# Performance work log

Measured on AMD Instinct MI355X. Metric: run time of the kernel, lower is better.

## Reference

```python
import jax, jax.numpy as jnp
import numpy as np


def gcn_conv(x, W, b, src, dst):
    """PyG-style GCNConv: add self-loops, symmetric normalization, then scatter-add."""
    n = x.shape[0]
    loop = jnp.arange(n, dtype=src.dtype)
    s = jnp.concatenate([src, loop])  # [E+N]
    d = jnp.concatenate([dst, loop])
    deg = jax.ops.segment_sum(jnp.ones(s.shape[0], dtype=x.dtype), d, num_segments=n)
    dinv = jax.lax.rsqrt(jnp.maximum(deg, 1.0))  # deg >= 1 due to self-loops
    norm = dinv[s] * dinv[d]                     # [E+N]
    h = x @ W                                    # [N, out]
    msg = h[s] * norm[:, None]                   # gather + scale
    return jax.ops.segment_sum(msg, d, num_segments=n) + b


def setup_inputs() -> dict:
    key = jax.random.key(0)
    ks = jax.random.split(key, 8)
    N, E, IN, H, C = 50000, 800000, 128, 64, 16
    x = jax.random.normal(ks[0], (N, IN), dtype=jnp.float32)
    edge_index = jax.random.randint(ks[1], (2, E), 0, N, dtype=jnp.int32)
    def glorot(k, shp):
        fan_in, fan_out = shp
        lim = (6.0 / (fan_in + fan_out)) ** 0.5
        return jax.random.uniform(k, shp, jnp.float32, -lim, lim)
    return {
        "x": x,
        "edge_index": edge_index,
        "W1": glorot(ks[2], (IN, H)), "b1": jnp.zeros((H,), jnp.float32),
        "W2": glorot(ks[3], (H, H)),  "b2": jnp.zeros((H,), jnp.float32),
        "Wm1": glorot(ks[4], (2 * H, H)), "bm1": jnp.zeros((H,), jnp.float32),
        "Wm2": glorot(ks[5], (H, C)),     "bm2": jnp.zeros((C,), jnp.float32),
    }


def reference(x, edge_index, W1, b1, W2, b2, Wm1, bm1, Wm2, bm2):
    src, dst = edge_index[0], edge_index[1]
    h = jax.nn.relu(gcn_conv(x, W1, b1, src, dst))
    # dropout is identity in eval mode
    h = jax.nn.relu(gcn_conv(h, W2, b2, src, dst))
    ef = jnp.concatenate([h[src], h[dst]], axis=1)  # [E, 2H]
    z = jax.nn.relu(ef @ Wm1 + bm1)
    return z @ Wm2 + bm2  # [E, numClasses]
```

## Files before the change

### kernel.cpp

```cpp
#include <hip/hip_runtime.h>
#include <hip/hip_bf16.h>

__global__ __launch_bounds__(256) void k_deg(const int* __restrict__ dst, int* __restrict__ deg, int E) {
    int e = blockIdx.x * 256 + threadIdx.x;
    if (e < E) atomicAdd(&deg[dst[e]], 1);
}

__global__ __launch_bounds__(256) void k_dinv(const int* __restrict__ deg, float* __restrict__ dinv, int N) {
    int n = blockIdx.x * 256 + threadIdx.x;
    if (n < N) dinv[n] = rsqrtf((float)(deg[n] + 1));
}

__global__ __launch_bounds__(256) void k_scan_sum(const int* __restrict__ deg, int* __restrict__ bsum, int N) {
    int n = blockIdx.x * 256 + threadIdx.x;
    int v = (n < N) ? deg[n] : 0;
#pragma unroll
    for (int o = 32; o > 0; o >>= 1) v += __shfl_down(v, o, 64);
    __shared__ int sh[4];
    if ((threadIdx.x & 63) == 0) sh[threadIdx.x >> 6] = v;
    __syncthreads();
    if (threadIdx.x == 0) bsum[blockIdx.x] = sh[0] + sh[1] + sh[2] + sh[3];
}

__global__ __launch_bounds__(256) void k_scan_off(int* __restrict__ bsum, int nb) {
    __shared__ int sh[256];
    int t = threadIdx.x;
    sh[t] = (t < nb) ? bsum[t] : 0;
    __syncthreads();
    for (int o = 1; o < 256; o <<= 1) {
        int y = (t >= o) ? sh[t - o] : 0;
        __syncthreads();
        sh[t] += y;
        __syncthreads();
    }
    if (t < nb) bsum[t] = (t == 0) ? 0 : sh[t - 1];
}

__global__ __launch_bounds__(256) void k_scan_write(const int* __restrict__ deg, const int* __restrict__ boff,
                                                    int* __restrict__ row_start, int* __restrict__ cursor, int N) {
    int n = blockIdx.x * 256 + threadIdx.x;
    int t = threadIdx.x, lane = t & 63, w = t >> 6;
    int v = (n < N) ? deg[n] : 0;
    int x = v;
#pragma unroll
    for (int o = 1; o < 64; o <<= 1) {
        int y = __shfl_up(x, o, 64);
        if (lane >= o) x += y;
    }
    __shared__ int wsum[4];
    if (lane == 63) wsum[w] = x;
    __syncthreads();
    int wo = 0;
#pragma unroll
    for (int i = 0; i < 4; ++i) wo += (i < w) ? wsum[i] : 0;
    int excl = boff[blockIdx.x] + wo + x - v;
    if (n < N) { row_start[n] = excl; cursor[n] = excl; }
    if (n == N - 1) row_start[N] = excl + v;
}

template <bool PAIR>
__global__ __launch_bounds__(256) void k_fill(const int* __restrict__ src, const int* __restrict__ dst,
                                              int* __restrict__ cursor, void* __restrict__ item, int E) {
    int e = blockIdx.x * 256 + threadIdx.x;
    if (e < E) {
        int d = dst[e];
        int pos = atomicAdd(&cursor[d], 1);
        if (PAIR) ((int2*)item)[pos] = make_int2(src[e], e);
        else      ((int*)item)[pos] = e;
    }
}

__global__ __launch_bounds__(256) void k_dvec(const int* __restrict__ rowst, int* __restrict__ dvec, int N) {
    int w = threadIdx.x >> 6, lane = threadIdx.x & 63;
    int d = blockIdx.x * 4 + w;
    if (d >= N) return;
    int beg = rowst[d], end = rowst[d + 1];
    for (int k = beg + lane; k < end; k += 64) dvec[k] = d;
}

__global__ __launch_bounds__(256) void k_tr(const float* __restrict__ in, float* __restrict__ outp, int R, int C) {
    int i = blockIdx.x * 256 + threadIdx.x;
    if (i < R * C) {
        int r = i / C, c = i % C;
        outp[(size_t)c * R + r] = in[(size_t)r * C + c];
    }
}

__global__ __launch_bounds__(256) void k_wpq(const float* __restrict__ Wm1, float* __restrict__ WPQ) {
    int i = blockIdx.x * 256 + threadIdx.x;
    if (i < 128 * 64) {
        int j = i >> 6, k = i & 63;
        WPQ[i] = (j < 64) ? Wm1[k * 64 + j] : Wm1[(64 + k) * 64 + (j - 64)];
    }
}

template <int K, bool RELU, bool BIAS, bool SCALE>
__global__ __launch_bounds__(256) void k_mm_slice(const float* __restrict__ X,
                                                  const float* __restrict__ WT,
                                                  const float* __restrict__ bias,
                                                  const float* __restrict__ dinv,
                                                  float* __restrict__ Y, int N) {
    int n = blockIdx.x * 256 + threadIdx.x;
    int j0 = blockIdx.y * 16;
    int nc = n < N ? n : N - 1;
    const float* xr = X + (size_t)nc * K;
    const float* wr = WT + (size_t)j0 * K;
    float acc[16];
#pragma unroll
    for (int j = 0; j < 16; ++j) acc[j] = BIAS ? bias[j0 + j] : 0.f;
#pragma unroll 1
    for (int k0 = 0; k0 < K; k0 += 8) {
        float ef[8];
        *(float4*)(ef)     = *(const float4*)(xr + k0);
        *(float4*)(ef + 4) = *(const float4*)(xr + k0 + 4);
        if (RELU) {
#pragma unroll
            for (int kk = 0; kk < 8; ++kk) ef[kk] = fmaxf(ef[kk], 0.f);
        }
#pragma unroll
        for (int j = 0; j < 16; ++j) {
#pragma unroll
            for (int kk = 0; kk < 8; ++kk)
                acc[j] = fmaf(ef[kk], wr[j * K + k0 + kk], acc[j]);
        }
    }
    if (n < N) {
        if (SCALE) {
            float dn = dinv[n];
#pragma unroll
            for (int j = 0; j < 16; ++j) acc[j] *= dn;
        }
        float4* yp = (float4*)(Y + (size_t)n * 64 + j0);
#pragma unroll
        for (int q = 0; q < 4; ++q) yp[q] = *(float4*)(acc + q * 4);
    }
}

__global__ __launch_bounds__(256) void k_pq_slice(const float* __restrict__ A2,
                                                  const float* __restrict__ WPQ,
                                                  const float* __restrict__ bm1,
                                                  float* __restrict__ Pb, float* __restrict__ Qb, int N) {
    int n = blockIdx.x * 256 + threadIdx.x;
    int j0g = blockIdx.y * 16;
    bool isP = j0g < 64;
    int jo = isP ? j0g : j0g - 64;
    float* Y = isP ? Pb : Qb;
    int nc = n < N ? n : N - 1;
    const float* xr = A2 + (size_t)nc * 64;
    const float* wr = WPQ + (size_t)j0g * 64;
    float acc[16];
#pragma unroll
    for (int j = 0; j < 16; ++j) acc[j] = isP ? bm1[jo + j] : 0.f;
#pragma unroll 1
    for (int k0 = 0; k0 < 64; k0 += 8) {
        float ef[8];
        *(float4*)(ef)     = *(const float4*)(xr + k0);
        *(float4*)(ef + 4) = *(const float4*)(xr + k0 + 4);
#pragma unroll
        for (int kk = 0; kk < 8; ++kk) ef[kk] = fmaxf(ef[kk], 0.f);
#pragma unroll
        for (int j = 0; j < 16; ++j)
#pragma unroll
            for (int kk = 0; kk < 8; ++kk)
                acc[j] = fmaf(ef[kk], wr[j * 64 + k0 + kk], acc[j]);
    }
    if (n < N) {
        float4* yp = (float4*)(Y + (size_t)n * 64 + jo);
#pragma unroll
        for (int q = 0; q < 4; ++q) yp[q] = *(float4*)(acc + q * 4);
    }
}

template <bool PAIR>
__global__ __launch_bounds__(256) void k_gather(const float* __restrict__ hs, const float* __restrict__ dinv,
                                                const int* __restrict__ row_start, const void* __restrict__ item,
                                                const int* __restrict__ srcArr,
                                                const float* __restrict__ bias,
                                                float* __restrict__ a, int N) {
    int w = threadIdx.x >> 6, lane = threadIdx.x & 63;
    int d = blockIdx.x * 4 + w;
    if (d >= N) return;
    int beg = row_start[d], end = row_start[d + 1];
    float dd = dinv[d];
    float acc = hs[(size_t)d * 64 + lane];
    int k = beg;
    for (; k + 8 <= end; k += 8) {
        int ss[8];
        if (PAIR) {
            const int2* it = (const int2*)item;
#pragma unroll
            for (int u = 0; u < 8; ++u) ss[u] = it[k + u].x;
        } else {
            const int* eid = (const int*)item;
            int ee[8];
#pragma unroll
            for (int u = 0; u < 8; ++u) ee[u] = eid[k + u];
#pragma unroll
            for (int u = 0; u < 8; ++u) ss[u] = srcArr[ee[u]];
        }
        float v[8];
#pragma unroll
        for (int u = 0; u < 8; ++u) v[u] = hs[(size_t)ss[u] * 64 + lane];
#pragma unroll
        for (int u = 0; u < 8; ++u) acc += v[u];
    }
    for (; k < end; ++k) {
        int s = PAIR ? ((const int2*)item)[k].x : srcArr[((const int*)item)[k]];
        acc += hs[(size_t)s * 64 + lane];
    }
    a[(size_t)d * 64 + lane] = fmaf(acc, dd, bias[lane]);
}

__global__ __launch_bounds__(256) void k_p_inplace(float* __restrict__ A2P,
                                                   const float* __restrict__ WPQ,
                                                   const float* __restrict__ bm1, int N) {
    int n = blockIdx.x * 256 + threadIdx.x;
    int nc = n < N ? n : N - 1;
    const float* xr = A2P + (size_t)nc * 64;
    float acc[64];
#pragma unroll
    for (int j = 0; j < 64; ++j) acc[j] = bm1[j];
#pragma unroll 1
    for (int k0 = 0; k0 < 64; k0 += 8) {
        float ef[8];
        *(float4*)(ef)     = *(const float4*)(xr + k0);
        *(float4*)(ef + 4) = *(const float4*)(xr + k0 + 4);
#pragma unroll
        for (int kk = 0; kk < 8; ++kk) ef[kk] = fmaxf(ef[kk], 0.f);
#pragma unroll
        for (int j = 0; j < 64; ++j)
#pragma unroll
            for (int kk = 0; kk < 8; ++kk)
                acc[j] = fmaf(ef[kk], WPQ[j * 64 + k0 + kk], acc[j]);
    }
    if (n < N) {
#pragma unroll
        for (int q = 0; q < 16; ++q)
            *(float4*)(A2P + (size_t)n * 64 + q * 4) = *(float4*)(acc + q * 4);
    }
}

__global__ __launch_bounds__(256) void k_edge_pq(const float* __restrict__ P,
                                                 const float* __restrict__ Q,
                                                 const int* __restrict__ src,
                                                 const int* __restrict__ dst,
                                                 const float* __restrict__ W2T,
                                                 const float* __restrict__ bm2,
                                                 float* __restrict__ out, int E) {
    int e = blockIdx.x * 256 + threadIdx.x;
    int ec = e < E ? e : E - 1;
    int s = src[ec], d = dst[ec];
    const float4* p4 = (const float4*)(P + (size_t)s * 64);
    const float4* q4 = (const float4*)(Q + (size_t)d * 64);
    float z[64];
#pragma unroll
    for (int c = 0; c < 16; ++c) {
        float4 a = p4[c], b = q4[c];
        z[c * 4 + 0] = fmaxf(a.x + b.x, 0.f);
        z[c * 4 + 1] = fmaxf(a.y + b.y, 0.f);
        z[c * 4 + 2] = fmaxf(a.z + b.z, 0.f);
        z[c * 4 + 3] = fmaxf(a.w + b.w, 0.f);
    }
    float o[16];
#pragma unroll
    for (int c = 0; c < 16; ++c) {
        float a = bm2[c];
#pragma unroll
        for (int j = 0; j < 64; ++j) a = fmaf(z[j], W2T[c * 64 + j], a);
        o[c] = a;
    }
    if (e < E) {
        float4* op = (float4*)(out + (size_t)e * 16);
#pragma unroll
        for (int q = 0; q < 4; ++q) op[q] = *(float4*)(o + q * 4);
    }
}

template <bool PAIR>
__global__ __launch_bounds__(256) void k_edge_csr(const float* __restrict__ P,
                                                  const float* __restrict__ Q,
                                                  const int* __restrict__ dvec,
                                                  const void* __restrict__ item,
                                                  const int* __restrict__ srcArr,
                                                  const float* __restrict__ W2T,
                                                  const float* __restrict__ bm2,
                                                  float* __restrict__ out, int E) {
    int i = blockIdx.x * 256 + threadIdx.x;
    int ic = i < E ? i : E - 1;
    int s, e;
    if (PAIR) {
        int2 pe = ((const int2*)item)[ic];
        s = pe.x; e = pe.y;
    } else {
        e = ((const int*)item)[ic];
        s = srcArr[e];
    }
    int d = dvec[ic];
    const float4* p4 = (const float4*)(P + (size_t)s * 64);
    const float4* q4 = (const float4*)(Q + (size_t)d * 64);
    float o[16];
#pragma unroll
    for (int t = 0; t < 16; ++t) o[t] = bm2[t];
#pragma unroll
    for (int c = 0; c < 16; ++c) {
        float4 a = p4[c], b = q4[c];
        float z0 = fmaxf(a.x + b.x, 0.f);
        float z1 = fmaxf(a.y + b.y, 0.f);
        float z2 = fmaxf(a.z + b.z, 0.f);
        float z3 = fmaxf(a.w + b.w, 0.f);
#pragma unroll
        for (int t = 0; t < 16; ++t) {
            o[t] = fmaf(z0, W2T[t * 64 + c * 4 + 0], o[t]);
            o[t] = fmaf(z1, W2T[t * 64 + c * 4 + 1], o[t]);
            o[t] = fmaf(z2, W2T[t * 64 + c * 4 + 2], o[t]);
            o[t] = fmaf(z3, W2T[t * 64 + c * 4 + 3], o[t]);
        }
    }
    if (i < E) {
        float4* op = (float4*)(out + (size_t)e * 16);
#pragma unroll
        for (int q = 0; q < 4; ++q) op[q] = *(float4*)(o + q * 4);
    }
}

extern "C" void kernel_launch(void* const* d_in, const int* in_sizes, int n_in,
                              void* d_out, int out_size, void* d_ws, size_t ws_size,
                              hipStream_t stream) {
    const float* x   = (const float*)d_in[0];
    const int* ei    = (const int*)d_in[1];
    const float* W1  = (const float*)d_in[2];
    const float* b1  = (const float*)d_in[3];
    const float* W2  = (const float*)d_in[4];
    const float* b2  = (const float*)d_in[5];
    const float* Wm1 = (const float*)d_in[6];
    const float* bm1 = (const float*)d_in[7];
    const float* Wm2 = (const float*)d_in[8];
    const float* bm2 = (const float*)d_in[9];
    float* out = (float*)d_out;

    const int H  = in_sizes[3];
    const int IN = in_sizes[2] / H;
    const int N  = in_sizes[0] / IN;
    const int E  = in_sizes[1] / 2;
    const int* src = ei;
    const int* dst = ei + E;

    auto al = [](size_t b) { return (b + 255) & ~(size_t)255; };
    char* ws = (char*)d_ws;

    const size_t wb     = al((size_t)IN * H * 4) + al((size_t)H * H * 4) + al((size_t)2 * H * H * 4) + al((size_t)H * 16 * 4);
    const size_t rowstB = al(((size_t)N + 1) * 4);
    const size_t nodeB  = al((size_t)N * 64 * 4);
    const size_t pairB  = al((size_t)E * 8);
    const size_t eidB   = al((size_t)E * 4);
    const size_t needA  = wb + rowstB + pairB + 3 * nodeB;
    const size_t needB  = wb + rowstB + eidB  + 3 * nodeB;

    const int tier = (needA <= ws_size) ? 0 : (needB <= ws_size) ? 1 : 2;

    float *W1T, *W2T, *WPQ, *Wm2T, *bufB, *Qbuf, *Pbuf, *dinv;
    int *deg, *rowst, *cursor, *bsum;
    void* item;
    float* bufA = (float*)d_out;
    bool slicedP = true;

    size_t off = 0;
    auto alc = [&](size_t b) { void* p = ws + off; off += al(b); return p; };

    if (tier <= 1) {
        W1T  = (float*)alc((size_t)IN * H * 4);
        W2T  = (float*)alc((size_t)H * H * 4);
        WPQ  = (float*)alc((size_t)2 * H * H * 4);
        Wm2T = (float*)alc((size_t)H * 16 * 4);
        rowst = (int*)alc(((size_t)N + 1) * 4);
        item  = alc(tier == 0 ? (size_t)E * 8 : (size_t)E * 4);
        bufB = (float*)alc((size_t)N * 64 * 4);
        Qbuf = (float*)alc((size_t)N * 64 * 4);
        Pbuf = (float*)alc((size_t)N * 64 * 4);
        char* pz = (char*)Pbuf;
        dinv   = (float*)pz;
        deg    = (int*)(pz + al((size_t)N * 4));
        cursor = (int*)(pz + 2 * al((size_t)N * 4));
        bsum   = (int*)(pz + 3 * al((size_t)N * 4));
    } else {
        dinv = (float*)alc((size_t)N * 4);
        W1T  = (float*)alc((size_t)IN * H * 4);
        W2T  = (float*)alc((size_t)H * H * 4);
        WPQ  = (float*)alc((size_t)2 * H * H * 4);
        Wm2T = (float*)alc((size_t)H * 16 * 4);
        bufB = (float*)alc((size_t)N * 64 * 4);
        Qbuf = (float*)alc((size_t)N * 64 * 4);
        float* PbufSep = (float*)alc((size_t)N * 64 * 4);
        slicedP = (off <= ws_size);
        Pbuf = slicedP ? PbufSep : bufB;
        char* qz = (char*)Qbuf;
        size_t qo = 0;
        deg    = (int*)(qz + qo); qo += al((size_t)N * 4);
        rowst  = (int*)(qz + qo); qo += al(((size_t)N + 1) * 4);
        cursor = (int*)(qz + qo); qo += al((size_t)N * 4);
        bsum   = (int*)(qz + qo); qo += al(1024);
        item   = (void*)(qz + qo);
    }

    const int NBn = (N + 255) / 256;
    const int NBe = (E + 255) / 256;
    const int NG  = (N + 3) / 4;

    hipMemsetAsync(deg, 0, (size_t)N * sizeof(int), stream);
    k_deg<<<NBe, 256, 0, stream>>>(dst, deg, E);
    k_dinv<<<NBn, 256, 0, stream>>>(deg, dinv, N);
    k_scan_sum<<<NBn, 256, 0, stream>>>(deg, bsum, N);
    k_scan_off<<<1, 256, 0, stream>>>(bsum, NBn);
    k_scan_write<<<NBn, 256, 0, stream>>>(deg, bsum, rowst, cursor, N);
    if (tier == 1) k_fill<false><<<NBe, 256, 0, stream>>>(src, dst, cursor, item, E);
    else           k_fill<true ><<<NBe, 256, 0, stream>>>(src, dst, cursor, item, E);

    k_tr<<<(IN * H + 255) / 256, 256, 0, stream>>>(W1, W1T, IN, H);
    k_tr<<<(H * H + 255) / 256, 256, 0, stream>>>(W2, W2T, H, H);
    k_tr<<<(H * 16 + 255) / 256, 256, 0, stream>>>(Wm2, Wm2T, H, 16);
    k_wpq<<<(2 * H * H + 255) / 256, 256, 0, stream>>>(Wm1, WPQ);

    const dim3 G4(NBn, 4);
    const dim3 G8(NBn, 8);

    k_mm_slice<128, false, false, true><<<G4, 256, 0, stream>>>(x, W1T, nullptr, dinv, bufA, N);
    if (tier == 1) k_gather<false><<<NG, 256, 0, stream>>>(bufA, dinv, rowst, item, src, b1, bufB, N);
    else           k_gather<true ><<<NG, 256, 0, stream>>>(bufA, dinv, rowst, item, src, b1, bufB, N);

    k_mm_slice<64, true, false, true><<<G4, 256, 0, stream>>>(bufB, W2T, nullptr, dinv, bufA, N);
    if (tier == 1) k_gather<false><<<NG, 256, 0, stream>>>(bufA, dinv, rowst, item, src, b2, bufB, N);
    else           k_gather<true ><<<NG, 256, 0, stream>>>(bufA, dinv, rowst, item, src, b2, bufB, N);

    if (tier <= 1) {
        k_pq_slice<<<G8, 256, 0, stream>>>(bufB, WPQ, bm1, Pbuf, Qbuf, N);
        int* dvec = (int*)bufB;
        k_dvec<<<NG, 256, 0, stream>>>(rowst, dvec, N);
        if (tier == 0) k_edge_csr<true ><<<NBe, 256, 0, stream>>>(Pbuf, Qbuf, dvec, item, src, Wm2T, bm2, out, E);
        else           k_edge_csr<false><<<NBe, 256, 0, stream>>>(Pbuf, Qbuf, dvec, item, src, Wm2T, bm2, out, E);
    } else {
        k_mm_slice<64, true, false, false><<<G4, 256, 0, stream>>>(bufB, WPQ + 64 * 64, nullptr, nullptr, Qbuf, N);
        if (slicedP) k_mm_slice<64, true, true, false><<<G4, 256, 0, stream>>>(bufB, WPQ, bm1, nullptr, Pbuf, N);
        else         k_p_inplace<<<NBn, 256, 0, stream>>>(bufB, WPQ, bm1, N);
        k_edge_pq<<<NBe, 256, 0, stream>>>(Pbuf, Qbuf, src, dst, Wm2T, bm2, out, E);
    }
}
```

Baseline: 424.6 us.

## Stage gathered P rows through LDS with coalesced loads; fuse P/Q slice kernel

The edge kernel now loads each gathered P row cooperatively, with 16 threads per row doing float4 loads, into a 64KB LDS tile using a rotated layout to avoid bank conflicts. It then computes per-edge outputs from LDS instead of each thread reading a scattered 256B row on its own. The P/Q projection kernel computes matching P and Q column slices in one thread, which halves the grid and reuses each loaded input row twice. The cost is 64KB of LDS per block, which limits occupancy, an added block barrier, and higher register use in the fused projection.

Result: slower. 457.6 us (+7.8%).

```diff
diff --git a/kernel.cpp b/kernel.cpp
--- a/kernel.cpp
+++ b/kernel.cpp
@@ -141,16 +141,14 @@
                                                   const float* __restrict__ bm1,
                                                   float* __restrict__ Pb, float* __restrict__ Qb, int N) {
     int n = blockIdx.x * 256 + threadIdx.x;
-    int j0g = blockIdx.y * 16;
-    bool isP = j0g < 64;
-    int jo = isP ? j0g : j0g - 64;
-    float* Y = isP ? Pb : Qb;
+    int jo = blockIdx.y * 16;
     int nc = n < N ? n : N - 1;
     const float* xr = A2 + (size_t)nc * 64;
-    const float* wr = WPQ + (size_t)j0g * 64;
-    float acc[16];
-#pragma unroll
-    for (int j = 0; j < 16; ++j) acc[j] = isP ? bm1[jo + j] : 0.f;
+    const float* wp = WPQ + (size_t)jo * 64;
+    const float* wq = WPQ + (size_t)(64 + jo) * 64;
+    float ap[16], aq[16];
+#pragma unroll
+    for (int j = 0; j < 16; ++j) { ap[j] = bm1[jo + j]; aq[j] = 0.f; }
 #pragma unroll 1
     for (int k0 = 0; k0 < 64; k0 += 8) {
         float ef[8];
@@ -159,15 +157,22 @@
 #pragma unroll
         for (int kk = 0; kk < 8; ++kk) ef[kk] = fmaxf(ef[kk], 0.f);
 #pragma unroll
-        for (int j = 0; j < 16; ++j)
-#pragma unroll
-            for (int kk = 0; kk < 8; ++kk)
-                acc[j] = fmaf(ef[kk], wr[j * 64 + k0 + kk], acc[j]);
+        for (int j = 0; j < 16; ++j) {
+#pragma unroll
+            for (int kk = 0; kk < 8; ++kk) {
+                ap[j] = fmaf(ef[kk], wp[j * 64 + k0 + kk], ap[j]);
+                aq[j] = fmaf(ef[kk], wq[j * 64 + k0 + kk], aq[j]);
+            }
+        }
     }
     if (n < N) {
-        float4* yp = (float4*)(Y + (size_t)n * 64 + jo);
-#pragma unroll
-        for (int q = 0; q < 4; ++q) yp[q] = *(float4*)(acc + q * 4);
+        float4* pp = (float4*)(Pb + (size_t)n * 64 + jo);
+        float4* qp = (float4*)(Qb + (size_t)n * 64 + jo);
+#pragma unroll
+        for (int q = 0; q < 4; ++q) {
+            pp[q] = *(float4*)(ap + q * 4);
+            qp[q] = *(float4*)(aq + q * 4);
+        }
     }
 }
 
@@ -277,47 +282,57 @@
 }
 
 template <bool PAIR>
-__global__ __launch_bounds__(256) void k_edge_csr(const float* __restrict__ P,
-                                                  const float* __restrict__ Q,
-                                                  const int* __restrict__ dvec,
-                                                  const void* __restrict__ item,
-                                                  const int* __restrict__ srcArr,
-                                                  const float* __restrict__ W2T,
-                                                  const float* __restrict__ bm2,
-                                                  float* __restrict__ out, int E) {
-    int i = blockIdx.x * 256 + threadIdx.x;
-    int ic = i < E ? i : E - 1;
-    int s, e;
-    if (PAIR) {
-        int2 pe = ((const int2*)item)[ic];
-        s = pe.x; e = pe.y;
-    } else {
-        e = ((const int*)item)[ic];
-        s = srcArr[e];
-    }
-    int d = dvec[ic];
-    const float4* p4 = (const float4*)(P + (size_t)s * 64);
+__global__ __launch_bounds__(256) void k_edge_tile(const float* __restrict__ P,
+                                                   const float* __restrict__ Q,
+                                                   const int* __restrict__ dvec,
+                                                   const void* __restrict__ item,
+                                                   const int* __restrict__ srcArr,
+                                                   const float* __restrict__ W2T,
+                                                   const float* __restrict__ bm2,
+                                                   float* __restrict__ out, int E) {
+    __shared__ float ldsP[256 * 64];
+    const int t = threadIdx.x;
+    const int base = blockIdx.x * 256;
+    const int i = base + t;
+    const int ic = i < E ? i : E - 1;
+    int e_own;
+    if (PAIR) e_own = ((const int2*)item)[ic].y;
+    else      e_own = ((const int*)item)[ic];
+    const int d = dvec[ic];
+    const int g = t >> 4, c = t & 15;
+#pragma unroll 4
+    for (int it = 0; it < 16; ++it) {
+        int r = it * 16 + g;
+        int rc = (base + r) < E ? base + r : E - 1;
+        int sr;
+        if (PAIR) sr = ((const int2*)item)[rc].x;
+        else      sr = srcArr[((const int*)item)[rc]];
+        float4 v = *(const float4*)(P + (size_t)sr * 64 + c * 4);
+        *(float4*)(ldsP + r * 64 + (((c + r) & 15) << 2)) = v;
+    }
+    __syncthreads();
     const float4* q4 = (const float4*)(Q + (size_t)d * 64);
     float o[16];
 #pragma unroll
-    for (int t = 0; t < 16; ++t) o[t] = bm2[t];
-#pragma unroll
-    for (int c = 0; c < 16; ++c) {
-        float4 a = p4[c], b = q4[c];
-        float z0 = fmaxf(a.x + b.x, 0.f);
-        float z1 = fmaxf(a.y + b.y, 0.f);
-        float z2 = fmaxf(a.z + b.z, 0.f);
-        float z3 = fmaxf(a.w + b.w, 0.f);
-#pragma unroll
-        for (int t = 0; t < 16; ++t) {
-            o[t] = fmaf(z0, W2T[t * 64 + c * 4 + 0], o[t]);
-            o[t] = fmaf(z1, W2T[t * 64 + c * 4 + 1], o[t]);
-            o[t] = fmaf(z2, W2T[t * 64 + c * 4 + 2], o[t]);
-            o[t] = fmaf(z3, W2T[t * 64 + c * 4 + 3], o[t]);
+    for (int u = 0; u < 16; ++u) o[u] = bm2[u];
+#pragma unroll
+    for (int cc = 0; cc < 16; ++cc) {
+        float4 p = *(const float4*)(ldsP + t * 64 + (((cc + t) & 15) << 2));
+        float4 q = q4[cc];
+        float z0 = fmaxf(p.x + q.x, 0.f);
+        float z1 = fmaxf(p.y + q.y, 0.f);
+        float z2 = fmaxf(p.z + q.z, 0.f);
+        float z3 = fmaxf(p.w + q.w, 0.f);
+#pragma unroll
+        for (int u = 0; u < 16; ++u) {
+            o[u] = fmaf(z0, W2T[u * 64 + cc * 4 + 0], o[u]);
+            o[u] = fmaf(z1, W2T[u * 64 + cc * 4 + 1], o[u]);
+            o[u] = fmaf(z2, W2T[u * 64 + cc * 4 + 2], o[u]);
+            o[u] = fmaf(z3, W2T[u * 64 + cc * 4 + 3], o[u]);
         }
     }
     if (i < E) {
-        float4* op = (float4*)(out + (size_t)e * 16);
+        float4* op = (float4*)(out + (size_t)e_own * 16);
 #pragma unroll
         for (int q = 0; q < 4; ++q) op[q] = *(float4*)(o + q * 4);
     }
@@ -421,7 +436,6 @@
     k_wpq<<<(2 * H * H + 255) / 256, 256, 0, stream>>>(Wm1, WPQ);
 
     const dim3 G4(NBn, 4);
-    const dim3 G8(NBn, 8);
 
     k_mm_slice<128, false, false, true><<<G4, 256, 0, stream>>>(x, W1T, nullptr, dinv, bufA, N);
     if (tier == 1) k_gather<false><<<NG, 256, 0, stream>>>(bufA, dinv, rowst, item, src, b1, bufB, N);
@@ -432,11 +446,11 @@
     else           k_gather<true ><<<NG, 256, 0, stream>>>(bufA, dinv, rowst, item, src, b2, bufB, N);
 
     if (tier <= 1) {
-        k_pq_slice<<<G8, 256, 0, stream>>>(bufB, WPQ, bm1, Pbuf, Qbuf, N);
+        k_pq_slice<<<G4, 256, 0, stream>>>(bufB, WPQ, bm1, Pbuf, Qbuf, N);
         int* dvec = (int*)bufB;
         k_dvec<<<NG, 256, 0, stream>>>(rowst, dvec, N);
-        if (tier == 0) k_edge_csr<true ><<<NBe, 256, 0, stream>>>(Pbuf, Qbuf, dvec, item, src, Wm2T, bm2, out, E);
-        else           k_edge_csr<false><<<NBe, 256, 0, stream>>>(Pbuf, Qbuf, dvec, item, src, Wm2T, bm2, out, E);
+        if (tier == 0) k_edge_tile<true ><<<NBe, 256, 0, stream>>>(Pbuf, Qbuf, dvec, item, src, Wm2T, bm2, out, E);
+        else           k_edge_tile<false><<<NBe, 256, 0, stream>>>(Pbuf, Qbuf, dvec, item, src, Wm2T, bm2, out, E);
     } else {
         k_mm_slice<64, true, false, false><<<G4, 256, 0, stream>>>(bufB, WPQ + 64 * 64, nullptr, nullptr, Qbuf, N);
         if (slicedP) k_mm_slice<64, true, true, false><<<G4, 256, 0, stream>>>(bufB, WPQ, bm1, nullptr, Pbuf, N);
```
